# Optimization experiments

Hardware: AMD Instinct MI355X
Metric: run time of the kernel (lower is better)

## Reference

```python
import jax, jax.numpy as jnp
import numpy as np

NUM_HEADS = 16
ROPE_BASE = 10000.0


def _rotate_half(x):
    d = x.shape[-1] // 2
    return jnp.concatenate([-x[..., d:], x[..., :d]], axis=-1)


def _rope_cos_sin(seq_len, rot_dim, dtype):
    # LlamaRotaryEmbedding(dim=rot_dim): inv_freq over even indices, emb = cat(freqs, freqs)
    inv_freq = 1.0 / (ROPE_BASE ** (jnp.arange(0, rot_dim, 2, dtype=jnp.float32) / rot_dim))
    t = jnp.arange(seq_len, dtype=jnp.float32)
    freqs = t[:, None] * inv_freq[None, :]            # [S, rot_dim/2]
    emb = jnp.concatenate([freqs, freqs], axis=-1)    # [S, rot_dim]
    return jnp.cos(emb).astype(dtype), jnp.sin(emb).astype(dtype)


def setup_inputs() -> dict:
    key = jax.random.key(0)
    ks = jax.random.split(key, 9)
    B, S, H = 2, 2048, 2048
    L = H // 8
    s = 0.02
    return {
        "hidden_states": jax.random.normal(ks[0], (B, S, H), jnp.float32),
        "Wkv_d": jax.random.normal(ks[1], (H, L), jnp.float32) * s,
        "Wq_d": jax.random.normal(ks[2], (H, L), jnp.float32) * s,
        "Wk_u": jax.random.normal(ks[3], (L, H // 2), jnp.float32) * s,
        "Wq_u": jax.random.normal(ks[4], (L, H // 2), jnp.float32) * s,
        "Wv_u": jax.random.normal(ks[5], (L, H), jnp.float32) * s,
        "Wrk": jax.random.normal(ks[6], (H, H // 2), jnp.float32) * s,
        "Wrq": jax.random.normal(ks[7], (L, H // 2), jnp.float32) * s,
        "Wo": jax.random.normal(ks[8], (H, H), jnp.float32) * s,
    }


def reference(hidden_states, Wkv_d, Wq_d, Wk_u, Wq_u, Wv_u, Wrk, Wrq, Wo):
    B, S, H = hidden_states.shape
    nh = NUM_HEADS
    hd = H // nh          # 128
    rd = hd // 2          # 64 (rope / content half width)

    kv_d = hidden_states @ Wkv_d            # [B,S,L]
    q_d = hidden_states @ Wq_d              # [B,S,L]

    k_c = (kv_d @ Wk_u).reshape(B, S, nh, rd)
    q_c = (q_d @ Wq_u).reshape(B, S, nh, rd)
    v = (kv_d @ Wv_u).reshape(B, S, nh, hd)
    k_r = (hidden_states @ Wrk).reshape(B, S, nh, rd)
    q_r = (q_d @ Wrq).reshape(B, S, nh, rd)

    cos, sin = _rope_cos_sin(S, rd, hidden_states.dtype)
    cos = cos[None, :, None, :]             # [1,S,1,rd] broadcast over batch/heads
    sin = sin[None, :, None, :]
    q_r = q_r * cos + _rotate_half(q_r) * sin
    k_r = k_r * cos + _rotate_half(k_r) * sin

    q = jnp.concatenate([q_c, q_r], axis=-1).transpose(0, 2, 1, 3)  # [B,nh,S,hd]
    k = jnp.concatenate([k_c, k_r], axis=-1).transpose(0, 2, 1, 3)
    v = v.transpose(0, 2, 1, 3)

    scale = jnp.asarray(hd, q.dtype) ** -0.5
    scores = jnp.einsum("bhqd,bhkd->bhqk", q, k) * scale
    causal = jnp.tril(jnp.ones((S, S), dtype=bool))
    scores = jnp.where(causal[None, None], scores, jnp.finfo(scores.dtype).min)
    attn = jax.nn.softmax(scores, axis=-1)
    y = jnp.einsum("bhqk,bhkd->bhqd", attn, v)
    y = y.transpose(0, 2, 1, 3).reshape(B, S, H)
    return y @ Wo
```

## Files before the change

### kernel.cpp

```cpp
#include <hip/hip_runtime.h>
#include <hip/hip_bf16.h>
#include <math.h>


typedef __attribute__((ext_vector_type(8))) short bf16x8;
typedef __attribute__((ext_vector_type(4))) float f32x4;
typedef unsigned int u32;

#define MFMA16(a, b, c) __builtin_amdgcn_mfma_f32_16x16x32_bf16(a, b, c, 0, 0, 0)

__device__ __forceinline__ short f2bs(float f) {
  __hip_bfloat16 h = __float2bfloat16(f);
  return *reinterpret_cast<short*>(&h);
}
__device__ __forceinline__ float bs2f(short s) {
  union { unsigned int u; float f; } v;
  v.u = ((unsigned int)(unsigned short)s) << 16;
  return v.f;
}
__device__ __forceinline__ u32 fbits(float f) {
  union { float f; u32 u; } v; v.f = f; return v.u;
}

__device__ __forceinline__ void async16(const void* g, void* l) {
  __builtin_amdgcn_global_load_lds(
      (const __attribute__((address_space(1))) u32*)(unsigned long long)g,
      (__attribute__((address_space(3))) u32*)(unsigned int)(unsigned long long)l,
      16, 0, 0);
}
__device__ __forceinline__ void wait_vm0() {
  __builtin_amdgcn_s_waitcnt(0x0f70);
}

__device__ __forceinline__ void wtrans_tile(const float* __restrict__ W,
                                            short* __restrict__ Wt, int K, int N,
                                            int bx, int by, int tid) {
  __shared__ float t[32][33];
  int k0 = by * 32, n0 = bx * 32;
#pragma unroll
  for (int i = 0; i < 4; ++i) {
    int idx = tid + i * 256;
    int r = idx >> 5, c = idx & 31;
    t[r][c] = W[(size_t)(k0 + r) * N + n0 + c];
  }
  __syncthreads();
#pragma unroll
  for (int i = 0; i < 4; ++i) {
    int idx = tid + i * 256;
    int r = idx >> 5, c = idx & 31;
    Wt[(size_t)(n0 + r) * K + k0 + c] = f2bs(t[c][r]);
  }
}

__global__ __launch_bounds__(256) void prep_all(
    const float* __restrict__ hs, const float* __restrict__ Wkvd,
    const float* __restrict__ Wqd, const float* __restrict__ Wku,
    const float* __restrict__ Wqu, const float* __restrict__ Wvu,
    const float* __restrict__ Wrk, const float* __restrict__ Wrq,
    const float* __restrict__ Wo, short* __restrict__ hs_b,
    short* __restrict__ W1t, short* __restrict__ W2t,
    short* __restrict__ W3t, short* __restrict__ Wo_t) {
  const int b = blockIdx.x, tid = threadIdx.x;
  if (b < 8192) {
    int i = (b * 256 + tid) * 4;
    float4 v = *(const float4*)(hs + i);
    short4 o;
    o.x = f2bs(v.x); o.y = f2bs(v.y); o.z = f2bs(v.z); o.w = f2bs(v.w);
    *(short4*)(hs_b + i) = o;
  } else if (b < 8704) {
    int l = b - 8192; wtrans_tile(Wkvd, W1t, 2048, 256, l & 7, l >> 3, tid);
  } else if (b < 9216) {
    int l = b - 8704; wtrans_tile(Wqd, W1t + 256 * 2048, 2048, 256, l & 7, l >> 3, tid);
  } else if (b < 11264) {
    int l = b - 9216; wtrans_tile(Wrk, W1t + 512 * 2048, 2048, 1024, l & 31, l >> 5, tid);
  } else if (b < 11520) {
    int l = b - 11264; wtrans_tile(Wku, W2t, 256, 1024, l & 31, l >> 5, tid);
  } else if (b < 12032) {
    int l = b - 11520; wtrans_tile(Wvu, W2t + 1024 * 256, 256, 2048, l & 63, l >> 6, tid);
  } else if (b < 12288) {
    int l = b - 12032; wtrans_tile(Wqu, W3t, 256, 1024, l & 31, l >> 5, tid);
  } else if (b < 12544) {
    int l = b - 12288; wtrans_tile(Wrq, W3t + 1024 * 256, 256, 1024, l & 31, l >> 5, tid);
  } else {
    int l = b - 12544; wtrans_tile(Wo, Wo_t, 2048, 2048, l & 63, l >> 6, tid);
  }
}

__device__ __forceinline__ void cstore(float v, float* p) { *p = v; }
__device__ __forceinline__ void cstore(float v, short* p) { *p = f2bs(v); }

template <typename CT>
__global__ __launch_bounds__(256) void gemm_bt(const short* __restrict__ A, int lda,
                                               const short* __restrict__ Bt, int ldb,
                                               CT* __restrict__ C, int ldc, int K) {
  __shared__ short As[128 * 64];
  __shared__ short Bs[128 * 64];
  const int tid = threadIdx.x;
  const int wave = tid >> 6, lane = tid & 63;
  const int quad = lane >> 4, l15 = lane & 15;
  const int wm = wave & 1, wn = wave >> 1;
  const int row0 = blockIdx.y * 128, col0 = blockIdx.x * 128;
  const int sr = tid >> 3;
  const int sc = ((tid & 7) ^ (sr & 7)) * 8;
  const short* Ag = A + (size_t)(row0 + sr) * lda + sc;
  const short* Bg = Bt + (size_t)(col0 + sr) * ldb + sc;
  const int rk = l15 & 7;

  f32x4 acc[4][4];
#pragma unroll
  for (int i = 0; i < 4; ++i)
#pragma unroll
    for (int j = 0; j < 4; ++j) acc[i][j] = {0.f, 0.f, 0.f, 0.f};

  for (int k0 = 0; k0 < K; k0 += 64) {
    __syncthreads();
#pragma unroll
    for (int i = 0; i < 4; ++i) {
      async16(Ag + (size_t)(i * 32) * lda + k0, &As[i * 2048 + tid * 8]);
      async16(Bg + (size_t)(i * 32) * ldb + k0, &Bs[i * 2048 + tid * 8]);
    }
    wait_vm0();
    __syncthreads();
#pragma unroll
    for (int s = 0; s < 2; ++s) {
      bf16x8 af[4], bfr[4];
#pragma unroll
      for (int i = 0; i < 4; ++i) {
        af[i]  = *(const bf16x8*)&As[(wm * 64 + i * 16 + l15) * 64 +
                                     ((s * 4 + quad) ^ rk) * 8];
        bfr[i] = *(const bf16x8*)&Bs[(wn * 64 + i * 16 + l15) * 64 +
                                     ((s * 4 + quad) ^ rk) * 8];
      }
#pragma unroll
      for (int i = 0; i < 4; ++i)
#pragma unroll
        for (int j = 0; j < 4; ++j)
          acc[i][j] = MFMA16(af[i], bfr[j], acc[i][j]);
    }
  }
#pragma unroll
  for (int i = 0; i < 4; ++i)
#pragma unroll
    for (int j = 0; j < 4; ++j)
#pragma unroll
      for (int r = 0; r < 4; ++r) {
        int row = row0 + wm * 64 + i * 16 + quad * 4 + r;
        int col = col0 + wn * 64 + j * 16 + l15;
        cstore(acc[i][j][r], &C[(size_t)row * ldc + col]);
      }
}

__global__ __launch_bounds__(256) void gemm23(const short* __restrict__ C1,
                                              const short* __restrict__ W2t,
                                              short* __restrict__ C2,
                                              short* __restrict__ C3,
                                              short* __restrict__ vt) {
  __shared__ short As[128 * 64];
  __shared__ short Bs[128 * 64];
  const int tid = threadIdx.x;
  const int wave = tid >> 6, lane = tid & 63;
  const int quad = lane >> 4, l15 = lane & 15;
  const int wm = wave & 1, wn = wave >> 1;
  const int bx = blockIdx.x;
  const short* A = bx < 24 ? C1 : C1 + 256;
  const int row0 = blockIdx.y * 128;
  const int sr = tid >> 3;
  const int sc = ((tid & 7) ^ (sr & 7)) * 8;
  const short* Ag = A + (size_t)(row0 + sr) * 1536 + sc;
  const short* Bg = W2t + (size_t)(bx * 128 + sr) * 256 + sc;
  const int rk = l15 & 7;

  f32x4 acc[4][4];
#pragma unroll
  for (int i = 0; i < 4; ++i)
#pragma unroll
    for (int j = 0; j < 4; ++j) acc[i][j] = {0.f, 0.f, 0.f, 0.f};

  for (int k0 = 0; k0 < 256; k0 += 64) {
    __syncthreads();
#pragma unroll
    for (int i = 0; i < 4; ++i) {
      async16(Ag + (size_t)(i * 32) * 1536 + k0, &As[i * 2048 + tid * 8]);
      async16(Bg + (size_t)(i * 32) * 256 + k0, &Bs[i * 2048 + tid * 8]);
    }
    wait_vm0();
    __syncthreads();
#pragma unroll
    for (int s = 0; s < 2; ++s) {
      bf16x8 af[4], bfr[4];
#pragma unroll
      for (int i = 0; i < 4; ++i) {
        af[i]  = *(const bf16x8*)&As[(wm * 64 + i * 16 + l15) * 64 +
                                     ((s * 4 + quad) ^ rk) * 8];
        bfr[i] = *(const bf16x8*)&Bs[(wn * 64 + i * 16 + l15) * 64 +
                                     ((s * 4 + quad) ^ rk) * 8];
      }
#pragma unroll
      for (int i = 0; i < 4; ++i)
#pragma unroll
        for (int j = 0; j < 4; ++j)
          acc[i][j] = MFMA16(af[i], bfr[j], acc[i][j]);
    }
  }

  if (bx >= 8 && bx < 24) {
    const int b = row0 >> 11;
    const int s0 = row0 & 2047;
#pragma unroll
    for (int i = 0; i < 4; ++i)
#pragma unroll
      for (int j = 0; j < 4; ++j) {
        int vcol = (bx - 8) * 128 + wn * 64 + j * 16 + l15;
        int h = vcol >> 7, d = vcol & 127;
        int s = s0 + wm * 64 + i * 16 + quad * 4;
        short4 o;
        o.x = f2bs(acc[i][j][0]); o.y = f2bs(acc[i][j][1]);
        o.z = f2bs(acc[i][j][2]); o.w = f2bs(acc[i][j][3]);
        *(short4*)&vt[((size_t)((b * 16 + h) * 128 + d)) * 2048 + s] = o;
      }
  } else {
    short* C = bx < 8 ? C2 : C3;
    const int ldc = bx < 8 ? 1024 : 2048;
    const int colbase = bx < 8 ? bx * 128 : (bx - 24) * 128;
#pragma unroll
    for (int i = 0; i < 4; ++i)
#pragma unroll
      for (int j = 0; j < 4; ++j)
#pragma unroll
        for (int r = 0; r < 4; ++r) {
          int row = row0 + wm * 64 + i * 16 + quad * 4 + r;
          int col = colbase + wn * 64 + j * 16 + l15;
          C[(size_t)row * ldc + col] = f2bs(acc[i][j][r]);
        }
  }
}

__global__ __launch_bounds__(256) void rope_pack(
    const short* __restrict__ c3, const short* __restrict__ c2,
    const short* __restrict__ c1, short* __restrict__ qf,
    short* __restrict__ kf) {
  const float QSCALE = 0.08838834764831845f * 1.4426950408889634f;
  int idx = blockIdx.x * 256 + threadIdx.x;
  int m = idx >> 11;
  int col = idx & 2047;
  int h = col >> 7;
  int j = col & 127;
  int b = m >> 11, s = m & 2047;
  float oq, ok;
  if (j < 64) {
    oq = bs2f(c3[(size_t)m * 2048 + h * 64 + j]);
    ok = bs2f(c2[(size_t)m * 1024 + h * 64 + j]);
  } else {
    int jr = j - 64;
    int f = jr & 31;
    float ang = (float)s * __expf(-0.2878231366242557f * (float)f);
    float c = __cosf(ang), sn = __sinf(ang);
    size_t qb = (size_t)m * 2048 + 1024 + h * 64;
    size_t kb = (size_t)m * 1536 + 512 + h * 64;
    float xq = bs2f(c3[qb + jr]), xk = bs2f(c1[kb + jr]);
    float rq, rk;
    if (jr < 32) { rq = -bs2f(c3[qb + jr + 32]); rk = -bs2f(c1[kb + jr + 32]); }
    else         { rq =  bs2f(c3[qb + jr - 32]); rk =  bs2f(c1[kb + jr - 32]); }
    oq = fmaf(xq, c, rq * sn);
    ok = fmaf(xk, c, rk * sn);
  }
  size_t dst = (((size_t)b * 16 + h) * 2048 + s) * 128 + j;
  qf[dst] = f2bs(oq * QSCALE);
  kf[dst] = f2bs(ok);
}

__global__ __launch_bounds__(256) void attn_split(const short* __restrict__ qf,
                                                  const short* __restrict__ kf,
                                                  const short* __restrict__ vt,
                                                  short* __restrict__ part,
                                                  float2* __restrict__ ml) {
  __shared__ short Ks[2][32 * 128];
  __shared__ short Vs[2][128 * 32];
  __shared__ short Pw[4][16 * 32];
  const int lid = blockIdx.x;
  const int bh = (lid & 7) * 4 + ((lid >> 3) & 3);
  const int x  = lid >> 5;
  const int tid = threadIdx.x;
  const int wave = tid >> 6, lane = tid & 63;
  const int quad = lane >> 4, l15 = lane & 15;
  const int krow_l = tid >> 4;
  const int kcol_sw = ((tid & 15) ^ krow_l) * 8;
  const int vrow_l = tid >> 2;
  const int vcol_sw = ((tid & 3) ^ (vrow_l & 3) ^ ((vrow_l >> 2) & 3)) * 8;
  const short* kgB = kf + (((size_t)bh * 2048) + krow_l) * 128 + kcol_sw;
  const short* vgB = vt + ((size_t)bh * 128 + vrow_l) * 2048 + vcol_sw;
  const int pswz = l15 & 6;

  for (int pass = 0; pass < 2; ++pass) {
    const int qt = pass ? 31 - x : x;
    const int ks = pass ? qt + 1 : 0;
    const int ke = pass ? 2 * (qt + 1) : x + 1;
    const int q0w = qt * 64 + wave * 16;

    bf16x8 qfr[4];
    {
      const short* qp = qf + (((size_t)bh * 2048) + q0w + l15) * 128;
#pragma unroll
      for (int kc = 0; kc < 4; ++kc)
        qfr[kc] = *(const bf16x8*)(qp + kc * 32 + quad * 8);
    }
    float m_i = -INFINITY;
    float l_i = 0.f;
    f32x4 O[8];
#pragma unroll
    for (int dt = 0; dt < 8; ++dt) O[dt] = {0.f, 0.f, 0.f, 0.f};

    {
      const short* kg = kgB + (size_t)ks * 32 * 128;
      const short* vg = vgB + ks * 32;
#pragma unroll
      for (int i = 0; i < 2; ++i) {
        async16(kg + (size_t)i * 16 * 128, &Ks[0][i * 2048 + tid * 8]);
        async16(vg + (size_t)i * 64 * 2048, &Vs[0][i * 2048 + tid * 8]);
      }
    }
    wait_vm0();
    __syncthreads();

    int cur = 0;
    for (int kt = ks; kt < ke; ++kt) {
      const int k0 = kt * 32;
      if (kt + 1 < ke) {
        const short* kg = kgB + (size_t)(kt + 1) * 32 * 128;
        const short* vg = vgB + (kt + 1) * 32;
#pragma unroll
        for (int i = 0; i < 2; ++i) {
          async16(kg + (size_t)i * 16 * 128, &Ks[cur ^ 1][i * 2048 + tid * 8]);
          async16(vg + (size_t)i * 64 * 2048, &Vs[cur ^ 1][i * 2048 + tid * 8]);
        }
      }

      f32x4 St[2];
#pragma unroll
      for (int j = 0; j < 2; ++j) St[j] = {0.f, 0.f, 0.f, 0.f};
      __builtin_amdgcn_s_setprio(1);
#pragma unroll
      for (int kc = 0; kc < 4; ++kc) {
        bf16x8 kb[2];
#pragma unroll
        for (int j = 0; j < 2; ++j)
          kb[j] = *(const bf16x8*)&Ks[cur][(j * 16 + l15) * 128 +
                                          (((kc * 4 + quad) ^ l15) & 15) * 8];
#pragma unroll
        for (int j = 0; j < 2; ++j)
          St[j] = MFMA16(kb[j], qfr[kc], St[j]);
      }
      __builtin_amdgcn_s_setprio(0);

      if (kt >= 2 * qt) {
#pragma unroll
        for (int j = 0; j < 2; ++j)
#pragma unroll
          for (int r = 0; r < 4; ++r)
            if (k0 + j * 16 + quad * 4 + r > q0w + l15)
              St[j][r] = -INFINITY;
      }

      {
        float mt = -INFINITY;
#pragma unroll
        for (int j = 0; j < 2; ++j)
#pragma unroll
          for (int r = 0; r < 4; ++r) mt = fmaxf(mt, St[j][r]);
        if (!__all(mt <= m_i + 8.f)) {
          mt = fmaxf(mt, __shfl_xor(mt, 16));
          mt = fmaxf(mt, __shfl_xor(mt, 32));
          float mnew = fmaxf(m_i, mt);
          float a = __builtin_amdgcn_exp2f(m_i - mnew);
          m_i = mnew;
          l_i *= a;
#pragma unroll
          for (int dt = 0; dt < 8; ++dt)
#pragma unroll
            for (int r = 0; r < 4; ++r) O[dt][r] *= a;
        }
        float ms = (m_i == -INFINITY) ? 0.f : m_i;
        float ps = 0.f;
#pragma unroll
        for (int j = 0; j < 2; ++j)
#pragma unroll
          for (int r = 0; r < 4; ++r) {
            float p = __builtin_amdgcn_exp2f(St[j][r] - ms);
            St[j][r] = p;
            ps += p;
          }
        l_i += ps;
      }

      {
        int pr = l15;
#pragma unroll
        for (int j = 0; j < 2; ++j) {
          u32 u0 = (fbits(St[j][1]) & 0xffff0000u) | (fbits(St[j][0]) >> 16);
          u32 u1 = (fbits(St[j][3]) & 0xffff0000u) | (fbits(St[j][2]) >> 16);
          uint2 pk; pk.x = u0; pk.y = u1;
          int g = (j * 4 + quad) ^ pswz;
          *(uint2*)&Pw[wave][pr * 32 + g * 4] = pk;
        }
      }

      __builtin_amdgcn_s_setprio(1);
      bf16x8 pa;
      {
        int g = (quad * 2) ^ pswz;
        pa = *(const bf16x8*)&Pw[wave][l15 * 32 + g * 4];
      }
#pragma unroll
      for (int dt = 0; dt < 8; ++dt) {
        bf16x8 vb = *(const bf16x8*)&Vs[cur][(dt * 16 + l15) * 32 +
                                            ((quad ^ (l15 & 3) ^ ((l15 >> 2) & 3)) & 3) * 8];
        O[dt] = MFMA16(vb, pa, O[dt]);
      }
      __builtin_amdgcn_s_setprio(0);

      wait_vm0();
      __syncthreads();
      cur ^= 1;
    }

    const int pidx = (bh * 32 + qt) * 2 + pass;
    short* pb = part + (size_t)pidx * 64 * 128;
    {
      int qrow = wave * 16 + l15;
#pragma unroll
      for (int dt = 0; dt < 8; ++dt) {
        short4 o;
        o.x = f2bs(O[dt][0]); o.y = f2bs(O[dt][1]);
        o.z = f2bs(O[dt][2]); o.w = f2bs(O[dt][3]);
        *(short4*)&pb[(size_t)qrow * 128 + dt * 16 + quad * 4] = o;
      }
    }
    float lr = l_i;
    lr += __shfl_xor(lr, 16);
    lr += __shfl_xor(lr, 32);
    if (quad == 0) {
      float2 v; v.x = m_i; v.y = lr;
      ml[pidx * 64 + wave * 16 + l15] = v;
    }
  }
}

__global__ __launch_bounds__(256) void attn_merge(const short* __restrict__ part,
                                                  const float2* __restrict__ ml,
                                                  short* __restrict__ y) {
  const int l = blockIdx.x;
  const int bh = ((l & 7) << 2) | ((l >> 3) & 3);
  const int qt = (l >> 5) & 31;
  const int b = bh >> 4, h = bh & 15;
  const int row = threadIdx.x >> 2, d0 = (threadIdx.x & 3) * 32;
  const int p1 = (bh * 32 + qt) * 2, p2 = p1 + 1;
  float2 a = ml[p1 * 64 + row], c = ml[p2 * 64 + row];
  float m = fmaxf(a.x, c.x);
  float a1 = __builtin_amdgcn_exp2f(a.x - m);
  float a2 = __builtin_amdgcn_exp2f(c.x - m);
  float invl = 1.f / (a.y * a1 + c.y * a2);
  a1 *= invl; a2 *= invl;
  const short* s1 = part + ((size_t)p1 * 64 + row) * 128 + d0;
  const short* s2 = part + ((size_t)p2 * 64 + row) * 128 + d0;
  short* yp = y + (((size_t)b * 2048 + qt * 64 + row) * 16 + h) * 128 + d0;
#pragma unroll
  for (int j = 0; j < 8; ++j) {
    short4 v1 = *(const short4*)(s1 + j * 4);
    short4 v2 = *(const short4*)(s2 + j * 4);
    short4 o;
    o.x = f2bs(bs2f(v1.x) * a1 + bs2f(v2.x) * a2);
    o.y = f2bs(bs2f(v1.y) * a1 + bs2f(v2.y) * a2);
    o.z = f2bs(bs2f(v1.z) * a1 + bs2f(v2.z) * a2);
    o.w = f2bs(bs2f(v1.w) * a1 + bs2f(v2.w) * a2);
    *(short4*)(yp + j * 4) = o;
  }
}

extern "C" void kernel_launch(void* const* d_in, const int* in_sizes, int n_in,
                              void* d_out, int out_size, void* d_ws, size_t ws_size,
                              hipStream_t stream) {
  const float* hs   = (const float*)d_in[0];
  const float* Wkvd = (const float*)d_in[1];
  const float* Wqd  = (const float*)d_in[2];
  const float* Wku  = (const float*)d_in[3];
  const float* Wqu  = (const float*)d_in[4];
  const float* Wvu  = (const float*)d_in[5];
  const float* Wrk  = (const float*)d_in[6];
  const float* Wrq  = (const float*)d_in[7];
  const float* Wo   = (const float*)d_in[8];
  float* out = (float*)d_out;
  char* ws = (char*)d_ws;
  const size_t MB = 1024ull * 1024ull;

  short* hs_b = (short*)(ws + 0 * MB);
  short* W1t  = (short*)(ws + 16 * MB);
  short* W2t  = (short*)(ws + 22 * MB);
  short* W3t  = W2t + 3072 * 256;
  short* C1   = (short*)(ws + 25 * MB);
  short* C2   = (short*)(ws + 37 * MB);
  short* C3   = (short*)(ws + 61 * MB);
  short* Wo_t = (short*)(ws + 77 * MB);
  short* q_f  = (short*)(ws + 85 * MB);
  short* k_f  = (short*)(ws + 101 * MB);
  short* v_t  = (short*)(ws + 117 * MB);
  short* y_b  = (short*)(ws + 133 * MB);
  short*  partb = (short*)(ws + 0 * MB);
  float2* mlb   = (float2*)(ws + 32 * MB);

  dim3 blk(256);
  prep_all<<<dim3(16640), blk, 0, stream>>>(hs, Wkvd, Wqd, Wku, Wqu, Wvu, Wrk,
                                            Wrq, Wo, hs_b, W1t, W2t, W3t, Wo_t);

  gemm_bt<short><<<dim3(12, 32), blk, 0, stream>>>(hs_b, 2048, W1t, 2048, C1, 1536, 2048);
  gemm23<<<dim3(40, 32), blk, 0, stream>>>(C1, W2t, C2, C3, v_t);

  rope_pack<<<dim3(32768), blk, 0, stream>>>(C3, C2, C1, q_f, k_f);

  attn_split<<<dim3(1024), blk, 0, stream>>>(q_f, k_f, v_t, partb, mlb);
  attn_merge<<<dim3(1024), blk, 0, stream>>>(partb, mlb, y_b);

  gemm_bt<float><<<dim3(16, 32), blk, 0, stream>>>(y_b, 2048, Wo_t, 2048, out, 2048, 2048);
}
```

Before: 329.0 us.

## Fuse RoPE and head-layout packing into GEMM epilogues; remap blocks across XCDs

The standalone rope_pack kernel is removed. RoPE, the softmax scale and the [b,h,s,d] packing are now applied directly in the epilogues of the first GEMM (k rope part) and of gemm23 (q content, q rope and k content). This avoids writing the C2/C3 intermediates and reading them back, and drops one kernel launch. C1 shrinks to a 512-wide buffer. It also adds an XCD-aware block-index remap so that neighbouring row tiles land on the same XCD for L2 reuse. The epilogue stores are scattered 2-byte writes, which may coalesce poorly.

```diff
diff --git a/kernel.cpp b/kernel.cpp
--- a/kernel.cpp
+++ b/kernel.cpp
@@ -8,6 +8,9 @@
 typedef unsigned int u32;
 
 #define MFMA16(a, b, c) __builtin_amdgcn_mfma_f32_16x16x32_bf16(a, b, c, 0, 0, 0)
+
+#define QSCALE_F (0.08838834764831845f * 1.4426950408889634f)
+#define ROPE_EXP (-0.2878231366242557f)
 
 __device__ __forceinline__ short f2bs(float f) {
   __hip_bfloat16 h = __float2bfloat16(f);
@@ -30,6 +33,14 @@
 }
 __device__ __forceinline__ void wait_vm0() {
   __builtin_amdgcn_s_waitcnt(0x0f70);
+}
+
+__device__ __forceinline__ void xcd_remap(int& bx, int& by) {
+  const int id = blockIdx.y * gridDim.x + blockIdx.x;
+  const int nyp = gridDim.y >> 3;
+  const int xcd = id & 7, t = id >> 3;
+  by = xcd * nyp + (t % nyp);
+  bx = t / nyp;
 }
 
 __device__ __forceinline__ void wtrans_tile(const float* __restrict__ W,
@@ -99,7 +110,8 @@
   const int wave = tid >> 6, lane = tid & 63;
   const int quad = lane >> 4, l15 = lane & 15;
   const int wm = wave & 1, wn = wave >> 1;
-  const int row0 = blockIdx.y * 128, col0 = blockIdx.x * 128;
+  int bx, by; xcd_remap(bx, by);
+  const int row0 = by * 128, col0 = bx * 128;
   const int sr = tid >> 3;
   const int sc = ((tid & 7) ^ (sr & 7)) * 8;
   const short* Ag = A + (size_t)(row0 + sr) * lda + sc;
@@ -150,10 +162,100 @@
       }
 }
 
+__global__ __launch_bounds__(256) void gemm1k(const short* __restrict__ A,
+                                              const short* __restrict__ Bt,
+                                              short* __restrict__ C1,
+                                              short* __restrict__ kf) {
+  __shared__ short As[128 * 64];
+  __shared__ short Bs[128 * 64];
+  const int tid = threadIdx.x;
+  const int wave = tid >> 6, lane = tid & 63;
+  const int quad = lane >> 4, l15 = lane & 15;
+  const int wm = wave & 1, wn = wave >> 1;
+  int bx, by; xcd_remap(bx, by);
+  const int row0 = by * 128, col0 = bx * 128;
+  const int sr = tid >> 3;
+  const int sc = ((tid & 7) ^ (sr & 7)) * 8;
+  const short* Ag = A + (size_t)(row0 + sr) * 2048 + sc;
+  const short* Bg = Bt + (size_t)(col0 + sr) * 2048 + sc;
+  const int rk = l15 & 7;
+
+  f32x4 acc[4][4];
+#pragma unroll
+  for (int i = 0; i < 4; ++i)
+#pragma unroll
+    for (int j = 0; j < 4; ++j) acc[i][j] = {0.f, 0.f, 0.f, 0.f};
+
+  for (int k0 = 0; k0 < 2048; k0 += 64) {
+    __syncthreads();
+#pragma unroll
+    for (int i = 0; i < 4; ++i) {
+      async16(Ag + (size_t)(i * 32) * 2048 + k0, &As[i * 2048 + tid * 8]);
+      async16(Bg + (size_t)(i * 32) * 2048 + k0, &Bs[i * 2048 + tid * 8]);
+    }
+    wait_vm0();
+    __syncthreads();
+#pragma unroll
+    for (int s = 0; s < 2; ++s) {
+      bf16x8 af[4], bfr[4];
+#pragma unroll
+      for (int i = 0; i < 4; ++i) {
+        af[i]  = *(const bf16x8*)&As[(wm * 64 + i * 16 + l15) * 64 +
+                                     ((s * 4 + quad) ^ rk) * 8];
+        bfr[i] = *(const bf16x8*)&Bs[(wn * 64 + i * 16 + l15) * 64 +
+                                     ((s * 4 + quad) ^ rk) * 8];
+      }
+#pragma unroll
+      for (int i = 0; i < 4; ++i)
+#pragma unroll
+        for (int j = 0; j < 4; ++j)
+          acc[i][j] = MFMA16(af[i], bfr[j], acc[i][j]);
+    }
+  }
+
+  if (bx < 4) {
+#pragma unroll
+    for (int i = 0; i < 4; ++i)
+#pragma unroll
+      for (int jj = 0; jj < 4; ++jj)
+#pragma unroll
+        for (int r = 0; r < 4; ++r) {
+          int row = row0 + wm * 64 + i * 16 + quad * 4 + r;
+          int col = col0 + wn * 64 + jj * 16 + l15;
+          C1[(size_t)row * 512 + col] = f2bs(acc[i][jj][r]);
+        }
+  } else {
+    const int colb = (bx - 4) * 128 + wn * 64 + l15;
+    const int h = colb >> 6;
+    const float ef0 = __expf(ROPE_EXP * (float)l15);
+    const float ef1 = __expf(ROPE_EXP * (float)(l15 + 16));
+#pragma unroll
+    for (int i = 0; i < 4; ++i)
+#pragma unroll
+      for (int r = 0; r < 4; ++r) {
+        int row = row0 + wm * 64 + i * 16 + quad * 4 + r;
+        int s = row & 2047, b = row >> 11;
+        float fs = (float)s;
+        float a0 = fs * ef0, a1 = fs * ef1;
+        float c0 = __cosf(a0), s0 = __sinf(a0);
+        float c1 = __cosf(a1), s1 = __sinf(a1);
+        float o0 = acc[i][0][r] * c0 - acc[i][2][r] * s0;
+        float o2 = acc[i][2][r] * c0 + acc[i][0][r] * s0;
+        float o1 = acc[i][1][r] * c1 - acc[i][3][r] * s1;
+        float o3 = acc[i][3][r] * c1 + acc[i][1][r] * s1;
+        short* kp = kf + (((size_t)(b * 16 + h) * 2048 + s) * 128 + 64 + l15);
+        kp[0]  = f2bs(o0);
+        kp[16] = f2bs(o1);
+        kp[32] = f2bs(o2);
+        kp[48] = f2bs(o3);
+      }
+  }
+}
+
 __global__ __launch_bounds__(256) void gemm23(const short* __restrict__ C1,
                                               const short* __restrict__ W2t,
-                                              short* __restrict__ C2,
-                                              short* __restrict__ C3,
+                                              short* __restrict__ qf,
+                                              short* __restrict__ kf,
                                               short* __restrict__ vt) {
   __shared__ short As[128 * 64];
   __shared__ short Bs[128 * 64];
@@ -161,12 +263,12 @@
   const int wave = tid >> 6, lane = tid & 63;
   const int quad = lane >> 4, l15 = lane & 15;
   const int wm = wave & 1, wn = wave >> 1;
-  const int bx = blockIdx.x;
+  int bx, by; xcd_remap(bx, by);
   const short* A = bx < 24 ? C1 : C1 + 256;
-  const int row0 = blockIdx.y * 128;
+  const int row0 = by * 128;
   const int sr = tid >> 3;
   const int sc = ((tid & 7) ^ (sr & 7)) * 8;
-  const short* Ag = A + (size_t)(row0 + sr) * 1536 + sc;
+  const short* Ag = A + (size_t)(row0 + sr) * 512 + sc;
   const short* Bg = W2t + (size_t)(bx * 128 + sr) * 256 + sc;
   const int rk = l15 & 7;
 
@@ -180,7 +282,7 @@
     __syncthreads();
 #pragma unroll
     for (int i = 0; i < 4; ++i) {
-      async16(Ag + (size_t)(i * 32) * 1536 + k0, &As[i * 2048 + tid * 8]);
+      async16(Ag + (size_t)(i * 32) * 512 + k0, &As[i * 2048 + tid * 8]);
       async16(Bg + (size_t)(i * 32) * 256 + k0, &Bs[i * 2048 + tid * 8]);
     }
     wait_vm0();
@@ -203,70 +305,73 @@
     }
   }
 
-  if (bx >= 8 && bx < 24) {
+  if (bx < 8) {
+    const int colb = bx * 128 + wn * 64 + l15;
+    const int h = colb >> 6;
+#pragma unroll
+    for (int i = 0; i < 4; ++i)
+#pragma unroll
+      for (int r = 0; r < 4; ++r) {
+        int row = row0 + wm * 64 + i * 16 + quad * 4 + r;
+        int s = row & 2047, b = row >> 11;
+        short* kp = kf + (((size_t)(b * 16 + h) * 2048 + s) * 128 + l15);
+#pragma unroll
+        for (int jj = 0; jj < 4; ++jj) kp[jj * 16] = f2bs(acc[i][jj][r]);
+      }
+  } else if (bx < 24) {
     const int b = row0 >> 11;
     const int s0 = row0 & 2047;
 #pragma unroll
     for (int i = 0; i < 4; ++i)
 #pragma unroll
-      for (int j = 0; j < 4; ++j) {
-        int vcol = (bx - 8) * 128 + wn * 64 + j * 16 + l15;
+      for (int jj = 0; jj < 4; ++jj) {
+        int vcol = (bx - 8) * 128 + wn * 64 + jj * 16 + l15;
         int h = vcol >> 7, d = vcol & 127;
         int s = s0 + wm * 64 + i * 16 + quad * 4;
         short4 o;
-        o.x = f2bs(acc[i][j][0]); o.y = f2bs(acc[i][j][1]);
-        o.z = f2bs(acc[i][j][2]); o.w = f2bs(acc[i][j][3]);
+        o.x = f2bs(acc[i][jj][0]); o.y = f2bs(acc[i][jj][1]);
+        o.z = f2bs(acc[i][jj][2]); o.w = f2bs(acc[i][jj][3]);
         *(short4*)&vt[((size_t)((b * 16 + h) * 128 + d)) * 2048 + s] = o;
       }
+  } else if (bx < 32) {
+    const int colb = (bx - 24) * 128 + wn * 64 + l15;
+    const int h = colb >> 6;
+#pragma unroll
+    for (int i = 0; i < 4; ++i)
+#pragma unroll
+      for (int r = 0; r < 4; ++r) {
+        int row = row0 + wm * 64 + i * 16 + quad * 4 + r;
+        int s = row & 2047, b = row >> 11;
+        short* qp = qf + (((size_t)(b * 16 + h) * 2048 + s) * 128 + l15);
+#pragma unroll
+        for (int jj = 0; jj < 4; ++jj) qp[jj * 16] = f2bs(acc[i][jj][r] * QSCALE_F);
+      }
   } else {
-    short* C = bx < 8 ? C2 : C3;
-    const int ldc = bx < 8 ? 1024 : 2048;
-    const int colbase = bx < 8 ? bx * 128 : (bx - 24) * 128;
+    const int colb = (bx - 32) * 128 + wn * 64 + l15;
+    const int h = colb >> 6;
+    const float ef0 = __expf(ROPE_EXP * (float)l15);
+    const float ef1 = __expf(ROPE_EXP * (float)(l15 + 16));
 #pragma unroll
     for (int i = 0; i < 4; ++i)
 #pragma unroll
-      for (int j = 0; j < 4; ++j)
-#pragma unroll
-        for (int r = 0; r < 4; ++r) {
-          int row = row0 + wm * 64 + i * 16 + quad * 4 + r;
-          int col = colbase + wn * 64 + j * 16 + l15;
-          C[(size_t)row * ldc + col] = f2bs(acc[i][j][r]);
-        }
-  }
-}
-
-__global__ __launch_bounds__(256) void rope_pack(
-    const short* __restrict__ c3, const short* __restrict__ c2,
-    const short* __restrict__ c1, short* __restrict__ qf,
-    short* __restrict__ kf) {
-  const float QSCALE = 0.08838834764831845f * 1.4426950408889634f;
-  int idx = blockIdx.x * 256 + threadIdx.x;
-  int m = idx >> 11;
-  int col = idx & 2047;
-  int h = col >> 7;
-  int j = col & 127;
-  int b = m >> 11, s = m & 2047;
-  float oq, ok;
-  if (j < 64) {
-    oq = bs2f(c3[(size_t)m * 2048 + h * 64 + j]);
-    ok = bs2f(c2[(size_t)m * 1024 + h * 64 + j]);
-  } else {
-    int jr = j - 64;
-    int f = jr & 31;
-    float ang = (float)s * __expf(-0.2878231366242557f * (float)f);
-    float c = __cosf(ang), sn = __sinf(ang);
-    size_t qb = (size_t)m * 2048 + 1024 + h * 64;
-    size_t kb = (size_t)m * 1536 + 512 + h * 64;
-    float xq = bs2f(c3[qb + jr]), xk = bs2f(c1[kb + jr]);
-    float rq, rk;
-    if (jr < 32) { rq = -bs2f(c3[qb + jr + 32]); rk = -bs2f(c1[kb + jr + 32]); }
-    else         { rq =  bs2f(c3[qb + jr - 32]); rk =  bs2f(c1[kb + jr - 32]); }
-    oq = fmaf(xq, c, rq * sn);
-    ok = fmaf(xk, c, rk * sn);
-  }
-  size_t dst = (((size_t)b * 16 + h) * 2048 + s) * 128 + j;
-  qf[dst] = f2bs(oq * QSCALE);
-  kf[dst] = f2bs(ok);
+      for (int r = 0; r < 4; ++r) {
+        int row = row0 + wm * 64 + i * 16 + quad * 4 + r;
+        int s = row & 2047, b = row >> 11;
+        float fs = (float)s;
+        float a0 = fs * ef0, a1 = fs * ef1;
+        float c0 = __cosf(a0), s0 = __sinf(a0);
+        float c1 = __cosf(a1), s1 = __sinf(a1);
+        float o0 = (acc[i][0][r] * c0 - acc[i][2][r] * s0) * QSCALE_F;
+        float o2 = (acc[i][2][r] * c0 + acc[i][0][r] * s0) * QSCALE_F;
+        float o1 = (acc[i][1][r] * c1 - acc[i][3][r] * s1) * QSCALE_F;
+        float o3 = (acc[i][3][r] * c1 + acc[i][1][r] * s1) * QSCALE_F;
+        short* qp = qf + (((size_t)(b * 16 + h) * 2048 + s) * 128 + 64 + l15);
+        qp[0]  = f2bs(o0);
+        qp[16] = f2bs(o1);
+        qp[32] = f2bs(o2);
+        qp[48] = f2bs(o3);
+      }
+  }
 }
 
 __global__ __launch_bounds__(256) void attn_split(const short* __restrict__ qf,
@@ -497,8 +602,6 @@
   short* W2t  = (short*)(ws + 22 * MB);
   short* W3t  = W2t + 3072 * 256;
   short* C1   = (short*)(ws + 25 * MB);
-  short* C2   = (short*)(ws + 37 * MB);
-  short* C3   = (short*)(ws + 61 * MB);
   short* Wo_t = (short*)(ws + 77 * MB);
   short* q_f  = (short*)(ws + 85 * MB);
   short* k_f  = (short*)(ws + 101 * MB);
@@ -511,10 +614,8 @@
   prep_all<<<dim3(16640), blk, 0, stream>>>(hs, Wkvd, Wqd, Wku, Wqu, Wvu, Wrk,
                                             Wrq, Wo, hs_b, W1t, W2t, W3t, Wo_t);
 
-  gemm_bt<short><<<dim3(12, 32), blk, 0, stream>>>(hs_b, 2048, W1t, 2048, C1, 1536, 2048);
-  gemm23<<<dim3(40, 32), blk, 0, stream>>>(C1, W2t, C2, C3, v_t);
-
-  rope_pack<<<dim3(32768), blk, 0, stream>>>(C3, C2, C1, q_f, k_f);
+  gemm1k<<<dim3(12, 32), blk, 0, stream>>>(hs_b, W1t, C1, k_f);
+  gemm23<<<dim3(40, 32), blk, 0, stream>>>(C1, W2t, q_f, k_f, v_t);
 
   attn_split<<<dim3(1024), blk, 0, stream>>>(q_f, k_f, v_t, partb, mlb);
   attn_merge<<<dim3(1024), blk, 0, stream>>>(partb, mlb, y_b);
```

New measurement: 315.3 us. -4.2%, faster.
